# Kernel tuning notes

Hardware: AMD Instinct MI355X
Metric: run time of the kernel (lower is better)

The kernel has to match this reference:

```python
import jax, jax.numpy as jnp
import numpy as np

VOCAB = 100000
N_NODES = 200000
D = 128


def setup_inputs() -> dict:
    key = jax.random.key(0)
    k1, k2, k3, k4, k5, k6 = jax.random.split(key, 6)
    nodes = jax.random.randint(k1, (N_NODES,), 0, VOCAB, dtype=jnp.int64 if jax.config.jax_enable_x64 else jnp.int32).astype(jnp.int32)
    c2e_weight = jax.random.normal(k2, (VOCAB, D), dtype=jnp.float32)
    w1 = jax.random.normal(k3, (D, D), dtype=jnp.float32) * (1.0 / np.sqrt(D))
    b1 = jax.random.normal(k4, (D,), dtype=jnp.float32) * 0.01
    w2 = jax.random.normal(k5, (D, D), dtype=jnp.float32) * (1.0 / np.sqrt(D))
    b2 = jax.random.normal(k6, (D,), dtype=jnp.float32) * 0.01
    return {"nodes": nodes, "c2e_weight": c2e_weight, "w1": w1, "b1": b1, "w2": w2, "b2": b2}


def reference(nodes, c2e_weight, w1, b1, w2, b2):
    # Vectorized version of the per-node Python loop:
    #   ce = c2e.weight[node]; x = relu(w_r1(ce)); out = relu(w_r2(x))
    ce = c2e_weight[nodes]                         # [N, D] gather
    h = jax.nn.relu(ce @ w1.T + b1)                # [N, D]
    out = jax.nn.relu(h @ w2.T + b2)               # [N, D]
    return out
```

## Files before the change

kernel.cpp:

```cpp
#include <hip/hip_runtime.h>
#include <hip/hip_bf16.h>

#define D_DIM   128
#define MT      32
#define NBLOCKS 768
#define NTHR    256

typedef __attribute__((ext_vector_type(8))) short bf16x8;
typedef __attribute__((ext_vector_type(4))) float f32x4;

__device__ __forceinline__ unsigned short f2bf(float f) {
    return __builtin_bit_cast(unsigned short, __float2bfloat16(f));
}

__device__ __forceinline__ int sw_off(int row, int col) {
    return row * 128 + ((((col >> 3) ^ (row & 15)) << 3) | (col & 7));
}

__device__ __forceinline__ bf16x8 load_wfrag(const float* __restrict__ w, int j, int kb) {
    const float4 lo = *(const float4*)(w + j * D_DIM + kb);
    const float4 hi = *(const float4*)(w + j * D_DIM + kb + 4);
    bf16x8 r;
    r[0] = (short)f2bf(lo.x); r[1] = (short)f2bf(lo.y);
    r[2] = (short)f2bf(lo.z); r[3] = (short)f2bf(lo.w);
    r[4] = (short)f2bf(hi.x); r[5] = (short)f2bf(hi.y);
    r[6] = (short)f2bf(hi.z); r[7] = (short)f2bf(hi.w);
    return r;
}

__global__ __launch_bounds__(NTHR, 3)
void ctx_encoder(const int* __restrict__ nodes,
                 const float* __restrict__ c2e,
                 const float* __restrict__ w1,
                 const float* __restrict__ b1,
                 const float* __restrict__ w2,
                 const float* __restrict__ b2,
                 float* __restrict__ out,
                 int N) {
    __shared__ unsigned short sA[MT * 128];
    __shared__ unsigned short sH[MT * 128];

    const int t    = threadIdx.x;
    const int lane = t & 63;
    const int wave = t >> 6;
    const int cl   = lane & 15;
    const int quad = lane >> 4;

    const int grow0 = t >> 3;
    const int gc    = t & 7;

    bf16x8 wB1[2][4], wB2[2][4];
    float bias1[2], bias2[2];
    #pragma unroll
    for (int c = 0; c < 2; ++c) {
        const int j = (wave * 2 + c) * 16 + cl;
        bias1[c] = b1[j];
        bias2[c] = b2[j];
        #pragma unroll
        for (int ks = 0; ks < 4; ++ks) {
            const int kb = ks * 32 + quad * 8;
            wB1[c][ks] = load_wfrag(w1, j, kb);
            wB2[c][ks] = load_wfrag(w2, j, kb);
        }
    }

    const int nTiles = (N + MT - 1) / MT;
    int tl = blockIdx.x;

    int r0 = tl * MT + grow0;  r0 = r0 < N ? r0 : N - 1;
    int idx_cur = nodes[r0];
    float4 g[4];
    {
        const float* rp = c2e + (size_t)idx_cur * D_DIM + gc * 4;
        #pragma unroll
        for (int i = 0; i < 4; ++i)
            g[i] = *(const float4*)(rp + i * 32);
    }
    int idx_nxt = 0;
    if (tl + NBLOCKS < nTiles) {
        int r1 = (tl + NBLOCKS) * MT + grow0;  r1 = r1 < N ? r1 : N - 1;
        idx_nxt = nodes[r1];
    }

    while (tl < nTiles) {
        #pragma unroll
        for (int i = 0; i < 4; ++i) {
            ushort4 b;
            b.x = f2bf(g[i].x); b.y = f2bf(g[i].y);
            b.z = f2bf(g[i].z); b.w = f2bf(g[i].w);
            *(ushort4*)&sA[sw_off(grow0, gc * 4 + i * 32)] = b;
        }
        __syncthreads();

        bf16x8 aF[2][4];
        #pragma unroll
        for (int m = 0; m < 2; ++m)
            #pragma unroll
            for (int ks = 0; ks < 4; ++ks)
                aF[m][ks] = *(const bf16x8*)&sA[sw_off(m * 16 + cl, ks * 32 + quad * 8)];

        const int tn = tl + NBLOCKS;
        if (tn < nTiles) {
            const float* rp = c2e + (size_t)idx_nxt * D_DIM + gc * 4;
            #pragma unroll
            for (int i = 0; i < 4; ++i)
                g[i] = *(const float4*)(rp + i * 32);
            if (tn + NBLOCKS < nTiles) {
                int rn = (tn + NBLOCKS) * MT + grow0;  rn = rn < N ? rn : N - 1;
                idx_nxt = nodes[rn];
            }
        }

        #pragma unroll
        for (int m = 0; m < 2; ++m) {
            #pragma unroll
            for (int c = 0; c < 2; ++c) {
                f32x4 acc = {0.f, 0.f, 0.f, 0.f};
                #pragma unroll
                for (int ks = 0; ks < 4; ++ks)
                    acc = __builtin_amdgcn_mfma_f32_16x16x32_bf16(aF[m][ks], wB1[c][ks], acc, 0, 0, 0);
                const int j = (wave * 2 + c) * 16 + cl;
                #pragma unroll
                for (int r = 0; r < 4; ++r) {
                    float h = acc[r] + bias1[c];
                    h = h > 0.f ? h : 0.f;
                    sH[sw_off(m * 16 + quad * 4 + r, j)] = f2bf(h);
                }
            }
        }
        __syncthreads();

        bf16x8 hF[2][4];
        #pragma unroll
        for (int m = 0; m < 2; ++m)
            #pragma unroll
            for (int ks = 0; ks < 4; ++ks)
                hF[m][ks] = *(const bf16x8*)&sH[sw_off(m * 16 + cl, ks * 32 + quad * 8)];

        const size_t obase = (size_t)tl * MT;
        #pragma unroll
        for (int m = 0; m < 2; ++m) {
            #pragma unroll
            for (int c = 0; c < 2; ++c) {
                f32x4 acc = {0.f, 0.f, 0.f, 0.f};
                #pragma unroll
                for (int ks = 0; ks < 4; ++ks)
                    acc = __builtin_amdgcn_mfma_f32_16x16x32_bf16(hF[m][ks], wB2[c][ks], acc, 0, 0, 0);
                const int j = (wave * 2 + c) * 16 + cl;
                #pragma unroll
                for (int r = 0; r < 4; ++r) {
                    float o = acc[r] + bias2[c];
                    o = o > 0.f ? o : 0.f;
                    const long grow = (long)(obase + m * 16 + quad * 4 + r);
                    if (grow < N)
                        __builtin_nontemporal_store(o, &out[(size_t)grow * D_DIM + j]);
                }
            }
        }

        tl += NBLOCKS;
    }
}

extern "C" void kernel_launch(void* const* d_in, const int* in_sizes, int n_in,
                              void* d_out, int out_size, void* d_ws, size_t ws_size,
                              hipStream_t stream) {
    const int*   nodes = (const int*)d_in[0];
    const float* c2e   = (const float*)d_in[1];
    const float* w1    = (const float*)d_in[2];
    const float* b1    = (const float*)d_in[3];
    const float* w2    = (const float*)d_in[4];
    const float* b2    = (const float*)d_in[5];
    float* out = (float*)d_out;
    const int N = in_sizes[0];

    ctx_encoder<<<dim3(NBLOCKS), dim3(NTHR), 0, stream>>>(nodes, c2e, w1, b1, w2, b2, out, N);
}
```

Before: 181.3 us.

## Use 64-row tiles with 8 waves each owning one 16-column output slice

The block grows to 512 threads (8 waves) and the tile to 64 rows, with fewer persistent blocks. Each wave now holds weight fragments for one 16-column slice instead of two, which halves the per-thread weight registers. A fragments are loaded per m-block rather than all up front, so register pressure drops and occupancy can rise. Output stores switch from nontemporal to normal stores, which changes how the write stream is cached.

New measurement: 165.6 us. 1.1x faster.

```diff
diff --git a/kernel.cpp b/kernel.cpp
--- a/kernel.cpp
+++ b/kernel.cpp
@@ -2,9 +2,9 @@
 #include <hip/hip_bf16.h>
 
 #define D_DIM   128
-#define MT      32
-#define NBLOCKS 768
-#define NTHR    256
+#define MT      64
+#define NBLOCKS 512
+#define NTHR    512
 
 typedef __attribute__((ext_vector_type(8))) short bf16x8;
 typedef __attribute__((ext_vector_type(4))) float f32x4;
@@ -28,7 +28,7 @@
     return r;
 }
 
-__global__ __launch_bounds__(NTHR, 3)
+__global__ __launch_bounds__(NTHR, 4)
 void ctx_encoder(const int* __restrict__ nodes,
                  const float* __restrict__ c2e,
                  const float* __restrict__ w1,
@@ -45,24 +45,20 @@
     const int wave = t >> 6;
     const int cl   = lane & 15;
     const int quad = lane >> 4;
+    const int j    = wave * 16 + cl;
 
     const int grow0 = t >> 3;
     const int gc    = t & 7;
 
-    bf16x8 wB1[2][4], wB2[2][4];
-    float bias1[2], bias2[2];
+    bf16x8 wB1[4], wB2[4];
     #pragma unroll
-    for (int c = 0; c < 2; ++c) {
-        const int j = (wave * 2 + c) * 16 + cl;
-        bias1[c] = b1[j];
-        bias2[c] = b2[j];
-        #pragma unroll
-        for (int ks = 0; ks < 4; ++ks) {
-            const int kb = ks * 32 + quad * 8;
-            wB1[c][ks] = load_wfrag(w1, j, kb);
-            wB2[c][ks] = load_wfrag(w2, j, kb);
-        }
+    for (int ks = 0; ks < 4; ++ks) {
+        const int kb = ks * 32 + quad * 8;
+        wB1[ks] = load_wfrag(w1, j, kb);
+        wB2[ks] = load_wfrag(w2, j, kb);
     }
+    const float bias1 = b1[j];
+    const float bias2 = b2[j];
 
     const int nTiles = (N + MT - 1) / MT;
     int tl = blockIdx.x;
@@ -92,13 +88,6 @@
         }
         __syncthreads();
 
-        bf16x8 aF[2][4];
-        #pragma unroll
-        for (int m = 0; m < 2; ++m)
-            #pragma unroll
-            for (int ks = 0; ks < 4; ++ks)
-                aF[m][ks] = *(const bf16x8*)&sA[sw_off(m * 16 + cl, ks * 32 + quad * 8)];
-
         const int tn = tl + NBLOCKS;
         if (tn < nTiles) {
             const float* rp = c2e + (size_t)idx_nxt * D_DIM + gc * 4;
@@ -112,49 +101,42 @@
         }
 
         #pragma unroll
-        for (int m = 0; m < 2; ++m) {
+        for (int m = 0; m < 4; ++m) {
+            bf16x8 aF[4];
             #pragma unroll
-            for (int c = 0; c < 2; ++c) {
-                f32x4 acc = {0.f, 0.f, 0.f, 0.f};
-                #pragma unroll
-                for (int ks = 0; ks < 4; ++ks)
-                    acc = __builtin_amdgcn_mfma_f32_16x16x32_bf16(aF[m][ks], wB1[c][ks], acc, 0, 0, 0);
-                const int j = (wave * 2 + c) * 16 + cl;
-                #pragma unroll
-                for (int r = 0; r < 4; ++r) {
-                    float h = acc[r] + bias1[c];
-                    h = h > 0.f ? h : 0.f;
-                    sH[sw_off(m * 16 + quad * 4 + r, j)] = f2bf(h);
-                }
+            for (int ks = 0; ks < 4; ++ks)
+                aF[ks] = *(const bf16x8*)&sA[sw_off(m * 16 + cl, ks * 32 + quad * 8)];
+            f32x4 acc = {0.f, 0.f, 0.f, 0.f};
+            #pragma unroll
+            for (int ks = 0; ks < 4; ++ks)
+                acc = __builtin_amdgcn_mfma_f32_16x16x32_bf16(aF[ks], wB1[ks], acc, 0, 0, 0);
+            #pragma unroll
+            for (int r = 0; r < 4; ++r) {
+                float h = acc[r] + bias1;
+                h = h > 0.f ? h : 0.f;
+                sH[sw_off(m * 16 + quad * 4 + r, j)] = f2bf(h);
             }
         }
         __syncthreads();
 
-        bf16x8 hF[2][4];
+        const size_t obase = (size_t)tl * MT;
         #pragma unroll
-        for (int m = 0; m < 2; ++m)
+        for (int m = 0; m < 4; ++m) {
+            bf16x8 hF[4];
             #pragma unroll
             for (int ks = 0; ks < 4; ++ks)
-                hF[m][ks] = *(const bf16x8*)&sH[sw_off(m * 16 + cl, ks * 32 + quad * 8)];
-
-        const size_t obase = (size_t)tl * MT;
-        #pragma unroll
-        for (int m = 0; m < 2; ++m) {
+                hF[ks] = *(const bf16x8*)&sH[sw_off(m * 16 + cl, ks * 32 + quad * 8)];
+            f32x4 acc = {0.f, 0.f, 0.f, 0.f};
             #pragma unroll
-            for (int c = 0; c < 2; ++c) {
-                f32x4 acc = {0.f, 0.f, 0.f, 0.f};
-                #pragma unroll
-                for (int ks = 0; ks < 4; ++ks)
-                    acc = __builtin_amdgcn_mfma_f32_16x16x32_bf16(hF[m][ks], wB2[c][ks], acc, 0, 0, 0);
-                const int j = (wave * 2 + c) * 16 + cl;
-                #pragma unroll
-                for (int r = 0; r < 4; ++r) {
-                    float o = acc[r] + bias2[c];
-                    o = o > 0.f ? o : 0.f;
-                    const long grow = (long)(obase + m * 16 + quad * 4 + r);
-                    if (grow < N)
-                        __builtin_nontemporal_store(o, &out[(size_t)grow * D_DIM + j]);
-                }
+            for (int ks = 0; ks < 4; ++ks)
+                acc = __builtin_amdgcn_mfma_f32_16x16x32_bf16(hF[ks], wB2[ks], acc, 0, 0, 0);
+            #pragma unroll
+            for (int r = 0; r < 4; ++r) {
+                float o = acc[r] + bias2;
+                o = o > 0.f ? o : 0.f;
+                const long grow = (long)(obase + m * 16 + quad * 4 + r);
+                if (grow < N)
+                    out[(size_t)grow * D_DIM + j] = o;
             }
         }
 
```
